# Optimization experiments

Hardware: AMD Instinct MI355X
Metric: run time of the kernel (lower is better)

The kernel has to match this reference:

```python
import jax, jax.numpy as jnp
import numpy as np

N, D, C = 8192, 512, 1000


def setup_inputs() -> dict:
    key = jax.random.key(0)
    k1, k2, k3 = jax.random.split(key, 3)
    features = jax.random.normal(k1, (N, D), dtype=jnp.float32)
    centers = jax.random.normal(k2, (C, D), dtype=jnp.float32)
    labels = jax.random.randint(k3, (N,), 0, C, dtype=jnp.int64)
    return {"features": features, "centers": centers, "labels": labels}


def _l2_normalize(x, axis=1, eps=1e-12):
    # matches torch F.normalize(p=2): x / max(||x||, eps)
    norm = jnp.sqrt(jnp.sum(x * x, axis=axis, keepdims=True))
    return x / jnp.maximum(norm, eps)


def reference(features, centers, labels):
    f = _l2_normalize(features, axis=1)          # [N, D]
    c = _l2_normalize(centers, axis=1)           # [C, D]
    centers_batch = c[labels]                    # [N, D]
    pos_distances = 1.0 - jnp.sum(f * centers_batch, axis=1)      # [N]
    neg_distances = 1.0 - jnp.matmul(f, f.T)                       # [N, N]
    losses = pos_distances[:, None] - neg_distances                # [N, N]
    diff_class = labels[:, None] != labels[None, :]                # [N, N]
    valid = diff_class & (losses > 0.0)                            # [N, N]
    losses = jnp.where(valid, losses, 0.0)
    num_valid_pairs = jnp.sum(valid, axis=1)                       # [N]
    num_valid_pairs = jnp.where(num_valid_pairs > 0, num_valid_pairs, 1)
    sample_losses = jnp.sum(losses, axis=1) / num_valid_pairs.astype(losses.dtype)
    num_valid_samples = jnp.sum(sample_losses > 0.0)
    loss = jnp.sum(sample_losses)
    loss = jnp.where(num_valid_samples > 0,
                     loss / num_valid_samples.astype(loss.dtype), loss)
    return loss
```

## Files before the change

kernel.cpp:

```cpp
#include <hip/hip_runtime.h>
#include <hip/hip_bf16.h>
#include <hip/hip_fp8.h>
#include <stdint.h>
#include <math.h>

#define N_ROWS 8192
#define DIM    512
#define BM     128
#define BK     64
#define NB     (N_ROWS / BM)
#define NTRI   (NB * (NB + 1) / 2)
#define NKT    (DIM / BK)

typedef float f32x4 __attribute__((ext_vector_type(4)));
typedef long  lng2  __attribute__((ext_vector_type(2)));


__global__ __launch_bounds__(256) void k_prep(const float* __restrict__ feats,
                                              const float* __restrict__ centers,
                                              const int* __restrict__ labels,
                                              unsigned char* __restrict__ f_q,
                                              float* __restrict__ posdot,
                                              float* __restrict__ Ssum,
                                              int* __restrict__ Kcnt) {
    const int row = blockIdx.x;
    const int t = threadIdx.x;
    const float* src = feats + (size_t)row * DIM;
    float v0 = src[t], v1 = src[t + 256];
    float ss = v0 * v0 + v1 * v1;
#pragma unroll
    for (int m = 1; m < 64; m <<= 1) ss += __shfl_xor(ss, m, 64);
    __shared__ float red[12];
    const int lane = t & 63, wid = t >> 6;
    if (lane == 0) red[wid] = ss;
    __syncthreads();
    const float tot = red[0] + red[1] + red[2] + red[3];
    const float scale = 1.0f / fmaxf(sqrtf(tot), 1e-12f);
    const float n0 = v0 * scale, n1 = v1 * scale;
    {
        __hip_fp8_e4m3 q0(n0), q1(n1);
#pragma unroll
        for (int j = 0; j < 2; ++j) {
            const int k  = t + j * 256;
            const int kt = k >> 6, k6 = k & 63;
            const int h  = (k6 >> 5) & 1;
            const int u  = (k6 >> 3) & 3;
            const int pos = kt * 64 + u * 16 + h * 8 + (k6 & 7);
            const unsigned char qb = (j == 0) ? *reinterpret_cast<const unsigned char*>(&q0)
                                              : *reinterpret_cast<const unsigned char*>(&q1);
            f_q[(size_t)row * DIM + pos] = qb;
        }
    }

    const int lab = labels[row];
    const float* c = centers + (size_t)lab * DIM;
    const float c0 = c[t], c1 = c[t + 256];
    float cc = c0 * c0 + c1 * c1;
    float d  = n0 * c0 + n1 * c1;
#pragma unroll
    for (int m = 1; m < 64; m <<= 1) {
        cc += __shfl_xor(cc, m, 64);
        d  += __shfl_xor(d, m, 64);
    }
    if (lane == 0) { red[4 + wid] = cc; red[8 + wid] = d; }
    __syncthreads();
    if (t == 0) {
        const float ctot = red[4] + red[5] + red[6] + red[7];
        const float dtot = red[8] + red[9] + red[10] + red[11];
        posdot[row] = dtot / fmaxf(sqrtf(ctot), 1e-12f);
        Ssum[row] = 0.0f;
        Kcnt[row] = 0;
    }
}

__global__ __launch_bounds__(256) void k_pair(const unsigned char* __restrict__ f_q,
                                              const int* __restrict__ labels,
                                              const float* __restrict__ pd,
                                              float* __restrict__ Ssum,
                                              int* __restrict__ Kcnt) {
    __shared__ __align__(16) unsigned char sA[3][BM * BK];
    __shared__ __align__(16) unsigned char sB[3][BM * BK];
    __shared__ int   s_lr[BM];
    __shared__ int   s_lc[BM];
    __shared__ float s_pd[BM];
    __shared__ float s_pc[BM];

    const int tid  = threadIdx.x;
    const int lane = tid & 63;
    const int wid  = tid >> 6;
    const int wr   = wid >> 1, wc = wid & 1;

    const int t = blockIdx.x;
    int bi = (int)floor((2.0 * NB + 1.0 - sqrt((2.0 * NB + 1.0) * (2.0 * NB + 1.0) - 8.0 * (double)t)) * 0.5);
    while (bi * NB - bi * (bi - 1) / 2 > t) --bi;
    while ((bi + 1) * NB - (bi + 1) * bi / 2 <= t) ++bi;
    const int bj = bi + (t - (bi * NB - bi * (bi - 1) / 2));
    const int rowBase = bi * BM;
    const int colBase = bj * BM;
    const bool offdiag = (bi != bj);

    if (tid < BM) {
        s_lr[tid] = labels[rowBase + tid];
        s_pd[tid] = pd[rowBase + tid];
    } else {
        s_lc[tid - BM] = labels[colBase + tid - BM];
        s_pc[tid - BM] = pd[colBase + tid - BM];
    }

    f32x4 acc[4][4] = {};

    const int srow = lane >> 2;
    const int slu  = (lane & 3) ^ ((lane >> 3) & 3);

#define STAGE(KT, P)                                                                       \
    do {                                                                                   \
        const int k0_ = (KT) * BK;                                                         \
        _Pragma("unroll")                                                                  \
        for (int i_ = 0; i_ < 2; ++i_) {                                                   \
            const int ch_ = wid * 2 + i_;                                                  \
            const int r_  = ch_ * 16 + srow;                                               \
            const unsigned char* gA_ = f_q + ((size_t)(rowBase + r_) * DIM + k0_ + slu * 16); \
            const unsigned char* gB_ = f_q + ((size_t)(colBase + r_) * DIM + k0_ + slu * 16); \
            __builtin_amdgcn_global_load_lds(                                              \
                (const __attribute__((address_space(1))) void*)gA_,                        \
                (__attribute__((address_space(3))) void*)(&sA[P][ch_ * 1024]), 16, 0, 0);  \
            __builtin_amdgcn_global_load_lds(                                              \
                (const __attribute__((address_space(1))) void*)gB_,                        \
                (__attribute__((address_space(3))) void*)(&sB[P][ch_ * 1024]), 16, 0, 0);  \
        }                                                                                  \
    } while (0)

    const int pu = (lane >> 4) ^ ((lane >> 1) & 3);

#define COMPUTE(P)                                                                         \
    do {                                                                                   \
        lng2 aF[4], bF[4];                                                                 \
        _Pragma("unroll")                                                                  \
        for (int m = 0; m < 4; ++m) {                                                      \
            const int r = wr * 64 + m * 16 + (lane & 15);                                  \
            aF[m] = *(const lng2*)(&sA[P][r * 64 + pu * 16]);                              \
        }                                                                                  \
        _Pragma("unroll")                                                                  \
        for (int n = 0; n < 4; ++n) {                                                      \
            const int r = wc * 64 + n * 16 + (lane & 15);                                  \
            bF[n] = *(const lng2*)(&sB[P][r * 64 + pu * 16]);                              \
        }                                                                                  \
        _Pragma("unroll")                                                                  \
        for (int m = 0; m < 4; ++m)                                                        \
            _Pragma("unroll")                                                              \
            for (int n = 0; n < 4; ++n) {                                                  \
                acc[m][n] = __builtin_amdgcn_mfma_f32_16x16x32_fp8_fp8(aF[m].x, bF[n].x, acc[m][n], 0, 0, 0); \
                acc[m][n] = __builtin_amdgcn_mfma_f32_16x16x32_fp8_fp8(aF[m].y, bF[n].y, acc[m][n], 0, 0, 0); \
            }                                                                              \
    } while (0)

    STAGE(0, 0);
    STAGE(1, 1);
    asm volatile("s_waitcnt lgkmcnt(0)" ::: "memory");
    asm volatile("s_waitcnt vmcnt(4)" ::: "memory");
    __builtin_amdgcn_s_barrier();
    __builtin_amdgcn_sched_barrier(0);

    {
        int p0 = 0, p1 = 1, p2 = 2;
#pragma unroll
        for (int kt = 0; kt < NKT - 1; ++kt) {
            STAGE((kt + 2) & (NKT - 1), p2);
            COMPUTE(p0);
            asm volatile("s_waitcnt vmcnt(4)" ::: "memory");
            __builtin_amdgcn_s_barrier();
            __builtin_amdgcn_sched_barrier(0);
            const int tmp = p0; p0 = p1; p1 = p2; p2 = tmp;
        }
        COMPUTE(p0);
    }

#undef STAGE
#undef COMPUTE

    float colS[4] = {0.f, 0.f, 0.f, 0.f};
    int   colK[4] = {0, 0, 0, 0};
    int   lcv[4]; float pcv[4];
#pragma unroll
    for (int n = 0; n < 4; ++n) {
        const int jl = wc * 64 + n * 16 + (lane & 15);
        lcv[n] = s_lc[jl];
        pcv[n] = s_pc[jl];
    }

#pragma unroll
    for (int m = 0; m < 4; ++m) {
        float rowS[4] = {0.f, 0.f, 0.f, 0.f};
        int   rowK[4] = {0, 0, 0, 0};
        const int rbase = wr * 64 + m * 16 + ((lane >> 4) << 2);
        int myLr[4]; float myPd[4];
#pragma unroll
        for (int g = 0; g < 4; ++g) { myLr[g] = s_lr[rbase + g]; myPd[g] = s_pd[rbase + g]; }
#pragma unroll
        for (int n = 0; n < 4; ++n) {
#pragma unroll
            for (int g = 0; g < 4; ++g) {
                const float s = acc[m][n][g];
                const bool diff = (myLr[g] != lcv[n]);
                if (diff && s > myPd[g]) { rowS[g] += (s - myPd[g]); rowK[g] += 1; }
                if (offdiag && diff && s > pcv[n]) { colS[n] += (s - pcv[n]); colK[n] += 1; }
            }
        }
#pragma unroll
        for (int g = 0; g < 4; ++g) {
#pragma unroll
            for (int d = 1; d < 16; d <<= 1) {
                rowS[g] += __shfl_xor(rowS[g], d, 64);
                rowK[g] += __shfl_xor(rowK[g], d, 64);
            }
        }
        if ((lane & 15) == 0) {
#pragma unroll
            for (int g = 0; g < 4; ++g) {
                const int r = rowBase + rbase + g;
                atomicAdd(&Ssum[r], rowS[g]);
                atomicAdd(&Kcnt[r], rowK[g]);
            }
        }
    }

    if (offdiag) {
#pragma unroll
        for (int n = 0; n < 4; ++n) {
#pragma unroll
            for (int d = 16; d < 64; d <<= 1) {
                colS[n] += __shfl_xor(colS[n], d, 64);
                colK[n] += __shfl_xor(colK[n], d, 64);
            }
        }
        if (lane < 16) {
#pragma unroll
            for (int n = 0; n < 4; ++n) {
                const int c = colBase + wc * 64 + n * 16 + lane;
                atomicAdd(&Ssum[c], colS[n]);
                atomicAdd(&Kcnt[c], colK[n]);
            }
        }
    }
}

__global__ __launch_bounds__(1024) void k_final(const float* __restrict__ Ssum,
                                                const int* __restrict__ Kcnt,
                                                float* __restrict__ out) {
    const int t = threadIdx.x;
    double sum = 0.0; int cnt = 0;
    for (int i = t; i < N_ROWS; i += 1024) {
        const int k = Kcnt[i];
        if (k > 0) { sum += (double)Ssum[i] / (double)k; cnt += 1; }
    }
#pragma unroll
    for (int d = 1; d < 64; d <<= 1) {
        sum += __shfl_xor(sum, d, 64);
        cnt += __shfl_xor(cnt, d, 64);
    }
    __shared__ double s_sum[16];
    __shared__ int    s_cnt[16];
    const int lane = t & 63, wid = t >> 6;
    if (lane == 0) { s_sum[wid] = sum; s_cnt[wid] = cnt; }
    __syncthreads();
    if (t == 0) {
        double ts = 0.0; int tc = 0;
#pragma unroll
        for (int w = 0; w < 16; ++w) { ts += s_sum[w]; tc += s_cnt[w]; }
        out[0] = (float)(tc > 0 ? ts / (double)tc : ts);
    }
}

extern "C" void kernel_launch(void* const* d_in, const int* in_sizes, int n_in,
                              void* d_out, int out_size, void* d_ws, size_t ws_size,
                              hipStream_t stream) {
    const float* features = (const float*)d_in[0];
    const float* centers  = (const float*)d_in[1];
    const int*   labels   = (const int*)d_in[2];
    float* out = (float*)d_out;

    char* ws = (char*)d_ws;
    unsigned char* f_q    = (unsigned char*)(ws);
    float*         posdot = (float*)(ws + 0x400000);
    float*         Ssum   = (float*)(ws + 0x400000 + 0x8000);
    int*           Kcnt   = (int*)  (ws + 0x400000 + 0x10000);

    k_prep<<<N_ROWS, 256, 0, stream>>>(features, centers, labels, f_q, posdot, Ssum, Kcnt);
    k_pair<<<NTRI, 256, 0, stream>>>(f_q, labels, posdot, Ssum, Kcnt);
    k_final<<<1, 1024, 0, stream>>>(Ssum, Kcnt, out);
}
```

Baseline: 93.60 us.

## Switch pair kernel to double buffering and raise occupancy target

Cuts the LDS tile buffers from three stages to two and replaces the hand-scheduled triple-buffer pipeline (explicit waitcnt and sched_barrier) with a plain double-buffered loop using __syncthreads. The shared-memory label and posdot arrays are dropped, so epilogue values are read straight from global memory, and launch bounds now ask for 5 blocks per CU. The aim is lower LDS use and higher occupancy so more blocks can hide latency, at the cost of a shallower prefetch, full barriers that wait on every load, and possible register pressure from the occupancy hint.

```diff
diff --git a/kernel.cpp b/kernel.cpp
--- a/kernel.cpp
+++ b/kernel.cpp
@@ -73,17 +73,13 @@
     }
 }
 
-__global__ __launch_bounds__(256) void k_pair(const unsigned char* __restrict__ f_q,
-                                              const int* __restrict__ labels,
-                                              const float* __restrict__ pd,
-                                              float* __restrict__ Ssum,
-                                              int* __restrict__ Kcnt) {
-    __shared__ __align__(16) unsigned char sA[3][BM * BK];
-    __shared__ __align__(16) unsigned char sB[3][BM * BK];
-    __shared__ int   s_lr[BM];
-    __shared__ int   s_lc[BM];
-    __shared__ float s_pd[BM];
-    __shared__ float s_pc[BM];
+__global__ __launch_bounds__(256, 5) void k_pair(const unsigned char* __restrict__ f_q,
+                                                 const int* __restrict__ labels,
+                                                 const float* __restrict__ pd,
+                                                 float* __restrict__ Ssum,
+                                                 int* __restrict__ Kcnt) {
+    __shared__ __align__(16) unsigned char sA[2][BM * BK];
+    __shared__ __align__(16) unsigned char sB[2][BM * BK];
 
     const int tid  = threadIdx.x;
     const int lane = tid & 63;
@@ -98,14 +94,6 @@
     const int rowBase = bi * BM;
     const int colBase = bj * BM;
     const bool offdiag = (bi != bj);
-
-    if (tid < BM) {
-        s_lr[tid] = labels[rowBase + tid];
-        s_pd[tid] = pd[rowBase + tid];
-    } else {
-        s_lc[tid - BM] = labels[colBase + tid - BM];
-        s_pc[tid - BM] = pd[colBase + tid - BM];
-    }
 
     f32x4 acc[4][4] = {};
 
@@ -155,25 +143,15 @@
     } while (0)
 
     STAGE(0, 0);
-    STAGE(1, 1);
-    asm volatile("s_waitcnt lgkmcnt(0)" ::: "memory");
-    asm volatile("s_waitcnt vmcnt(4)" ::: "memory");
-    __builtin_amdgcn_s_barrier();
-    __builtin_amdgcn_sched_barrier(0);
-
-    {
-        int p0 = 0, p1 = 1, p2 = 2;
-#pragma unroll
-        for (int kt = 0; kt < NKT - 1; ++kt) {
-            STAGE((kt + 2) & (NKT - 1), p2);
-            COMPUTE(p0);
-            asm volatile("s_waitcnt vmcnt(4)" ::: "memory");
-            __builtin_amdgcn_s_barrier();
-            __builtin_amdgcn_sched_barrier(0);
-            const int tmp = p0; p0 = p1; p1 = p2; p2 = tmp;
-        }
-        COMPUTE(p0);
-    }
+    __syncthreads();
+
+    for (int kt = 0; kt < NKT - 1; ++kt) {
+        const int cur = kt & 1;
+        STAGE(kt + 1, cur ^ 1);
+        COMPUTE(cur);
+        __syncthreads();
+    }
+    COMPUTE((NKT - 1) & 1);
 
 #undef STAGE
 #undef COMPUTE
@@ -183,19 +161,19 @@
     int   lcv[4]; float pcv[4];
 #pragma unroll
     for (int n = 0; n < 4; ++n) {
-        const int jl = wc * 64 + n * 16 + (lane & 15);
-        lcv[n] = s_lc[jl];
-        pcv[n] = s_pc[jl];
+        const int jl = colBase + wc * 64 + n * 16 + (lane & 15);
+        lcv[n] = labels[jl];
+        pcv[n] = pd[jl];
     }
 
 #pragma unroll
     for (int m = 0; m < 4; ++m) {
         float rowS[4] = {0.f, 0.f, 0.f, 0.f};
         int   rowK[4] = {0, 0, 0, 0};
-        const int rbase = wr * 64 + m * 16 + ((lane >> 4) << 2);
+        const int rbase = rowBase + wr * 64 + m * 16 + ((lane >> 4) << 2);
         int myLr[4]; float myPd[4];
 #pragma unroll
-        for (int g = 0; g < 4; ++g) { myLr[g] = s_lr[rbase + g]; myPd[g] = s_pd[rbase + g]; }
+        for (int g = 0; g < 4; ++g) { myLr[g] = labels[rbase + g]; myPd[g] = pd[rbase + g]; }
 #pragma unroll
         for (int n = 0; n < 4; ++n) {
 #pragma unroll
@@ -217,9 +195,8 @@
         if ((lane & 15) == 0) {
 #pragma unroll
             for (int g = 0; g < 4; ++g) {
-                const int r = rowBase + rbase + g;
-                atomicAdd(&Ssum[r], rowS[g]);
-                atomicAdd(&Kcnt[r], rowK[g]);
+                atomicAdd(&Ssum[rbase + g], rowS[g]);
+                atomicAdd(&Kcnt[rbase + g], rowK[g]);
             }
         }
     }
```

Result: slower. 135.3 us (+44.5%).

## Enlarge pair-GEMM tile to 256x256 with 8 waves and 4-stage LDS pipeline

Applied to the files above, without the earlier changes.

Doubles the triangular block tile to 256 rows by 256 columns, uses 512 threads (2x4 waves, each computing a 128x64 sub-tile), and deepens the global-to-LDS pipeline from 3 to 4 stages with an explicit per-iteration wait schedule. MFMA blocks get s_setprio raised. The aim is to roughly halve global/LDS traffic per FLOP and cut block count and atomics, at the cost of more registers per wave (32 accumulators), 128KB LDS, and fewer blocks (528) to fill the GPU.

```diff
diff --git a/kernel.cpp b/kernel.cpp
--- a/kernel.cpp
+++ b/kernel.cpp
@@ -6,7 +6,7 @@
 
 #define N_ROWS 8192
 #define DIM    512
-#define BM     128
+#define BM     256
 #define BK     64
 #define NB     (N_ROWS / BM)
 #define NTRI   (NB * (NB + 1) / 2)
@@ -73,13 +73,13 @@
     }
 }
 
-__global__ __launch_bounds__(256) void k_pair(const unsigned char* __restrict__ f_q,
+__global__ __launch_bounds__(512) void k_pair(const unsigned char* __restrict__ f_q,
                                               const int* __restrict__ labels,
                                               const float* __restrict__ pd,
                                               float* __restrict__ Ssum,
                                               int* __restrict__ Kcnt) {
-    __shared__ __align__(16) unsigned char sA[3][BM * BK];
-    __shared__ __align__(16) unsigned char sB[3][BM * BK];
+    __shared__ __align__(16) unsigned char sA[4][BM * BK];
+    __shared__ __align__(16) unsigned char sB[4][BM * BK];
     __shared__ int   s_lr[BM];
     __shared__ int   s_lc[BM];
     __shared__ float s_pd[BM];
@@ -88,7 +88,8 @@
     const int tid  = threadIdx.x;
     const int lane = tid & 63;
     const int wid  = tid >> 6;
-    const int wr   = wid >> 1, wc = wid & 1;
+    const int wr   = wid >> 2;
+    const int wc   = wid & 3;
 
     const int t = blockIdx.x;
     int bi = (int)floor((2.0 * NB + 1.0 - sqrt((2.0 * NB + 1.0) * (2.0 * NB + 1.0) - 8.0 * (double)t)) * 0.5);
@@ -107,7 +108,7 @@
         s_pc[tid - BM] = pd[colBase + tid - BM];
     }
 
-    f32x4 acc[4][4] = {};
+    f32x4 acc[8][4] = {};
 
     const int srow = lane >> 2;
     const int slu  = (lane & 3) ^ ((lane >> 3) & 3);
@@ -132,51 +133,56 @@
 
     const int pu = (lane >> 4) ^ ((lane >> 1) & 3);
 
-#define COMPUTE(P)                                                                         \
-    do {                                                                                   \
-        lng2 aF[4], bF[4];                                                                 \
-        _Pragma("unroll")                                                                  \
-        for (int m = 0; m < 4; ++m) {                                                      \
-            const int r = wr * 64 + m * 16 + (lane & 15);                                  \
-            aF[m] = *(const lng2*)(&sA[P][r * 64 + pu * 16]);                              \
-        }                                                                                  \
-        _Pragma("unroll")                                                                  \
-        for (int n = 0; n < 4; ++n) {                                                      \
-            const int r = wc * 64 + n * 16 + (lane & 15);                                  \
-            bF[n] = *(const lng2*)(&sB[P][r * 64 + pu * 16]);                              \
-        }                                                                                  \
-        _Pragma("unroll")                                                                  \
-        for (int m = 0; m < 4; ++m)                                                        \
-            _Pragma("unroll")                                                              \
-            for (int n = 0; n < 4; ++n) {                                                  \
-                acc[m][n] = __builtin_amdgcn_mfma_f32_16x16x32_fp8_fp8(aF[m].x, bF[n].x, acc[m][n], 0, 0, 0); \
-                acc[m][n] = __builtin_amdgcn_mfma_f32_16x16x32_fp8_fp8(aF[m].y, bF[n].y, acc[m][n], 0, 0, 0); \
-            }                                                                              \
-    } while (0)
-
     STAGE(0, 0);
     STAGE(1, 1);
-    asm volatile("s_waitcnt lgkmcnt(0)" ::: "memory");
-    asm volatile("s_waitcnt vmcnt(4)" ::: "memory");
+    STAGE(2, 2);
+    asm volatile("s_waitcnt vmcnt(8)" ::: "memory");
     __builtin_amdgcn_s_barrier();
     __builtin_amdgcn_sched_barrier(0);
 
-    {
-        int p0 = 0, p1 = 1, p2 = 2;
-#pragma unroll
-        for (int kt = 0; kt < NKT - 1; ++kt) {
-            STAGE((kt + 2) & (NKT - 1), p2);
-            COMPUTE(p0);
+#pragma unroll
+    for (int kt = 0; kt < NKT; ++kt) {
+        const int P = kt & 3;
+        if (kt <= 4) STAGE(kt + 3, (kt + 3) & 3);
+
+        lng2 aF[8], bF[4];
+#pragma unroll
+        for (int m = 0; m < 8; ++m) {
+            const int r = wr * 128 + m * 16 + (lane & 15);
+            aF[m] = *(const lng2*)(&sA[P][r * 64 + pu * 16]);
+        }
+#pragma unroll
+        for (int n = 0; n < 4; ++n) {
+            const int r = wc * 64 + n * 16 + (lane & 15);
+            bF[n] = *(const lng2*)(&sB[P][r * 64 + pu * 16]);
+        }
+
+        __builtin_amdgcn_s_setprio(1);
+#pragma unroll
+        for (int m = 0; m < 8; ++m)
+#pragma unroll
+            for (int n = 0; n < 4; ++n) {
+                acc[m][n] = __builtin_amdgcn_mfma_f32_16x16x32_fp8_fp8(aF[m].x, bF[n].x, acc[m][n], 0, 0, 0);
+                acc[m][n] = __builtin_amdgcn_mfma_f32_16x16x32_fp8_fp8(aF[m].y, bF[n].y, acc[m][n], 0, 0, 0);
+            }
+        __builtin_amdgcn_s_setprio(0);
+
+        if (kt < 5) {
+            asm volatile("s_waitcnt vmcnt(8)" ::: "memory");
+            __builtin_amdgcn_s_barrier();
+            __builtin_amdgcn_sched_barrier(0);
+        } else if (kt == 5) {
             asm volatile("s_waitcnt vmcnt(4)" ::: "memory");
             __builtin_amdgcn_s_barrier();
             __builtin_amdgcn_sched_barrier(0);
-            const int tmp = p0; p0 = p1; p1 = p2; p2 = tmp;
-        }
-        COMPUTE(p0);
+        } else if (kt == 6) {
+            asm volatile("s_waitcnt vmcnt(0)" ::: "memory");
+            __builtin_amdgcn_s_barrier();
+            __builtin_amdgcn_sched_barrier(0);
+        }
     }
 
 #undef STAGE
-#undef COMPUTE
 
     float colS[4] = {0.f, 0.f, 0.f, 0.f};
     int   colK[4] = {0, 0, 0, 0};
@@ -189,13 +195,13 @@
     }
 
 #pragma unroll
-    for (int m = 0; m < 4; ++m) {
+    for (int m = 0; m < 8; ++m) {
         float rowS[4] = {0.f, 0.f, 0.f, 0.f};
         int   rowK[4] = {0, 0, 0, 0};
-        const int rbase = wr * 64 + m * 16 + ((lane >> 4) << 2);
+        const int rloc = wr * 128 + m * 16 + ((lane >> 4) << 2);
         int myLr[4]; float myPd[4];
 #pragma unroll
-        for (int g = 0; g < 4; ++g) { myLr[g] = s_lr[rbase + g]; myPd[g] = s_pd[rbase + g]; }
+        for (int g = 0; g < 4; ++g) { myLr[g] = s_lr[rloc + g]; myPd[g] = s_pd[rloc + g]; }
 #pragma unroll
         for (int n = 0; n < 4; ++n) {
 #pragma unroll
@@ -217,7 +223,7 @@
         if ((lane & 15) == 0) {
 #pragma unroll
             for (int g = 0; g < 4; ++g) {
-                const int r = rowBase + rbase + g;
+                const int r = rowBase + rloc + g;
                 atomicAdd(&Ssum[r], rowS[g]);
                 atomicAdd(&Kcnt[r], rowK[g]);
             }
@@ -286,6 +292,6 @@
     int*           Kcnt   = (int*)  (ws + 0x400000 + 0x10000);
 
     k_prep<<<N_ROWS, 256, 0, stream>>>(features, centers, labels, f_q, posdot, Ssum, Kcnt);
-    k_pair<<<NTRI, 256, 0, stream>>>(f_q, labels, posdot, Ssum, Kcnt);
+    k_pair<<<NTRI, 512, 0, stream>>>(f_q, labels, posdot, Ssum, Kcnt);
     k_final<<<1, 1024, 0, stream>>>(Ssum, Kcnt, out);
 }
```

Measured after the change: 103.0 us. 10.1% more time.
